# Kernel optimization log

Hardware: AMD Instinct MI355X
Metric: run time of the kernel (lower is better)

Reference implementation:

```python
import jax, jax.numpy as jnp
import numpy as np

B, T, D, H = 2, 2048, 1024, 16
DH = D // H


def setup_inputs() -> dict:
    key = jax.random.key(0)
    ks = jax.random.split(key, 5)
    scale = 1.0 / np.sqrt(D)
    return {
        "x": jax.random.normal(ks[0], (B, T, D), dtype=jnp.float32),
        "Wq": jax.random.normal(ks[1], (D, D), dtype=jnp.float32) * scale,
        "Wk": jax.random.normal(ks[2], (D, D), dtype=jnp.float32) * scale,
        "Wv": jax.random.normal(ks[3], (D, D), dtype=jnp.float32) * scale,
        "Wo": jax.random.normal(ks[4], (D, D), dtype=jnp.float32) * scale,
    }


def _split(y):
    # (B,T,D) -> (B,H,T,DH)
    b, t, _ = y.shape
    return y.reshape(b, t, H, DH).transpose(0, 2, 1, 3)


def reference(x, Wq, Wk, Wv, Wo):
    q = _split(x @ Wq)
    k = _split(x @ Wk)
    v = _split(x @ Wv)
    scores = jnp.einsum("bhqd,bhkd->bhqk", q, k) / jnp.sqrt(jnp.float32(DH))
    t = x.shape[1]
    # additive causal mask: -1e9 above the diagonal (matches band_part logic)
    causal = jnp.tril(jnp.ones((t, t), dtype=jnp.float32))
    scores = scores + (1.0 - causal) * -1e9
    attn = jax.nn.softmax(scores, axis=-1)
    out = jnp.einsum("bhqk,bhkd->bhqd", attn, v)  # (B,H,T,DH)
    out = out.transpose(0, 2, 1, 3).reshape(x.shape[0], t, D)
    return out @ Wo
```

## Files before the change

kernel.cpp:

```cpp
#include <hip/hip_runtime.h>

#define BB 2
#define TT 2048
#define DD 1024
#define HH 16
#define DHD 64
#define MM (BB*TT)

typedef __attribute__((ext_vector_type(8))) short short8;
typedef __attribute__((ext_vector_type(4))) float float4v;
typedef unsigned short u16;

__device__ inline float bf2f(u16 u) {
    union { unsigned int i; float f; } v;
    v.i = ((unsigned int)u) << 16;
    return v.f;
}
__device__ inline u16 f2bf(float f) {
    union { float f; unsigned int i; } v;
    v.f = f;
    unsigned int x = v.i;
    unsigned int r = (x + 0x7fffu + ((x >> 16) & 1u)) >> 16;
    return (u16)r;
}

__global__ __launch_bounds__(256) void prep_k(const float* __restrict__ x,
                                              const float* __restrict__ Wq,
                                              const float* __restrict__ Wk,
                                              const float* __restrict__ Wv,
                                              const float* __restrict__ Wo,
                                              u16* __restrict__ xb,
                                              u16* __restrict__ WT) {
    int tid = threadIdx.x;
    if (blockIdx.z == 4) {
        int bid = blockIdx.y * 32 + blockIdx.x;
#pragma unroll
        for (int k = 0; k < 4; k++) {
            int i = bid * 1024 + k * 256 + tid;
            float4v v = ((const float4v*)x)[i];
            ushort4 o;
            o.x = f2bf(v[0]); o.y = f2bf(v[1]); o.z = f2bf(v[2]); o.w = f2bf(v[3]);
            ((ushort4*)xb)[i] = o;
        }
        return;
    }
    __shared__ u16 t[32][33];
    int wsel = blockIdx.z;
    const float* W = (wsel == 0) ? Wq : (wsel == 1) ? Wk : (wsel == 2) ? Wv : Wo;
    u16* o = WT + (size_t)wsel * DD * DD;
    int k0 = blockIdx.y * 32, n0 = blockIdx.x * 32;
    int tx = tid & 31, ty = tid >> 5;
#pragma unroll
    for (int i = 0; i < 4; i++) {
        int k = ty + i * 8;
        t[k][tx] = f2bf(W[(size_t)(k0 + k) * DD + n0 + tx]);
    }
    __syncthreads();
#pragma unroll
    for (int i = 0; i < 4; i++) {
        int n = ty + i * 8;
        o[(size_t)(n0 + n) * DD + k0 + tx] = t[tx][n];
    }
}

template <int MODE, int TM, int TN, int BK>
__global__ __launch_bounds__(256) void gemm_k(const u16* __restrict__ A,
                                              const u16* __restrict__ WT0,
                                              void* __restrict__ outp) {
    const int K = DD;
    const int MT = TM / 32, NT = TN / 32;
    const int NS = (TM + TN) * (BK / 8) / 256;
    const int CPR = BK / 8;

    int z = blockIdx.z;
    const u16* WT = WT0 + (size_t)z * DD * DD;
    int n0 = blockIdx.x * TN, m0 = blockIdx.y * TM;

    __shared__ u16 S[(TM + TN) * BK];

    int tid = threadIdx.x;
    int lane = tid & 63, w = tid >> 6;
    int wm = (w >> 1) * (TM / 2), wn = (w & 1) * (TN / 2);
    int quad = lane >> 4, l16 = lane & 15;

    const u16* gp[NS];
    u16* lp[NS];
#pragma unroll
    for (int j = 0; j < NS; j++) {
        int cid = tid + j * 256;
        int r = cid / CPR, c = cid % CPR;
        lp[j] = S + r * BK + (c ^ (r & 7)) * 8;
        gp[j] = (r < TM ? A + (size_t)(m0 + r) * K
                        : WT + (size_t)(n0 + r - TM) * K) + c * 8;
    }
    int swz = l16 & 7;

    float4v acc[MT][NT];
#pragma unroll
    for (int i = 0; i < MT; i++)
#pragma unroll
        for (int j = 0; j < NT; j++) acc[i][j] = (float4v)(0.0f);

    short8 pr[NS];
#pragma unroll
    for (int j = 0; j < NS; j++) pr[j] = *(const short8*)gp[j];

    const int NK = K / BK;
#pragma unroll 1
    for (int ki = 0; ki < NK; ki++) {
        __syncthreads();
#pragma unroll
        for (int j = 0; j < NS; j++) *(short8*)lp[j] = pr[j];
        __syncthreads();

        if (ki + 1 < NK) {
            int k0 = (ki + 1) * BK;
#pragma unroll
            for (int j = 0; j < NS; j++) pr[j] = *(const short8*)(gp[j] + k0);
        }

#pragma unroll
        for (int ks = 0; ks < BK / 32; ks++) {
            int cq = ((ks * 4 + quad) ^ swz) * 8;
            short8 a[MT], b[NT];
#pragma unroll
            for (int mt = 0; mt < MT; mt++)
                a[mt] = *(const short8*)&S[(wm + mt * 16 + l16) * BK + cq];
#pragma unroll
            for (int nt = 0; nt < NT; nt++)
                b[nt] = *(const short8*)&S[(TM + wn + nt * 16 + l16) * BK + cq];
#pragma unroll
            for (int mt = 0; mt < MT; mt++)
#pragma unroll
                for (int nt = 0; nt < NT; nt++)
                    acc[mt][nt] = __builtin_amdgcn_mfma_f32_16x16x32_bf16(
                        a[mt], b[nt], acc[mt][nt], 0, 0, 0);
        }
    }

#pragma unroll
    for (int mt = 0; mt < MT; mt++) {
#pragma unroll
        for (int nt = 0; nt < NT; nt++) {
#pragma unroll
            for (int r = 0; r < 4; r++) {
                int m = m0 + wm + mt * 16 + quad * 4 + r;
                int n = n0 + wn + nt * 16 + l16;
                float v = acc[mt][nt][r];
                if constexpr (MODE == 0) {
                    int bb = m >> 11, t = m & 2047;
                    int h = n >> 6, dh = n & 63;
                    size_t idx;
                    if (z == 2)
                        idx = (((size_t)2 * BB * HH + bb * HH + h) * DHD + dh) * TT + t;
                    else
                        idx = (((size_t)z * BB * HH + bb * HH + h) * TT + t) * DHD + dh;
                    ((u16*)outp)[idx] = f2bf(v);
                } else {
                    ((float*)outp)[(size_t)m * DD + n] = v;
                }
            }
        }
    }
}

__global__ __launch_bounds__(512) void attn_k(const u16* __restrict__ QKV,
                                              u16* __restrict__ AO) {
    const u16* Q  = QKV;
    const u16* Kp = QKV + (size_t)MM * DD;
    const u16* Vp = QKV + (size_t)2 * MM * DD;
    int bh = blockIdx.x;
    int qt = 31 - blockIdx.y;
    size_t hoff = (size_t)bh * TT * DHD;

    __shared__ u16 Ks[2][2][64 * 64];
    __shared__ u16 VTs[2][2][64 * 64];
    __shared__ u16 Ps[8][16 * 64];

    int tid = threadIdx.x;
    int lane = tid & 63, wv = tid >> 6;
    int g = wv >> 2, w4 = wv & 3;
    int quad = lane >> 4, l16 = lane & 15;
    int cxs = l16 & 7;

    int sr = tid >> 3, sc = tid & 7;
    int sl = sr * 64 + ((sc ^ (sr & 7)) * 8);
    const u16* gK = Kp + hoff + (size_t)sr * DHD + sc * 8;
    const u16* gV = Vp + hoff + (size_t)sr * TT + sc * 8;

    u16* Qstage = &Ps[0][0];

    const float qscale = 0.125f * 1.4426950408889634f;
    int q0 = qt * 64;
    {
        short8 v = *(const short8*)(Q + hoff + (size_t)(q0 + sr) * DHD + sc * 8);
        short8 sv;
#pragma unroll
        for (int e = 0; e < 8; e++) sv[e] = (short)f2bf(bf2f((u16)v[e]) * qscale);
        *(short8*)&Qstage[sl] = sv;
    }

    short8 prK[2], prV[2];
    prK[0] = *(const short8*)gK;
    prK[1] = *(const short8*)(gK + (size_t)64 * DHD);
    prV[0] = *(const short8*)gV;
    prV[1] = *(const short8*)(gV + 64);

    __syncthreads();
    int fr = w4 * 16 + l16;
    short8 aq0 = *(const short8*)&Qstage[fr * 64 + ((quad ^ cxs) * 8)];
    short8 aq1 = *(const short8*)&Qstage[fr * 64 + (((4 + quad) ^ cxs) * 8)];

    int NR = (qt >> 1) + 1;

    float4v o[4];
#pragma unroll
    for (int i = 0; i < 4; i++) o[i] = (float4v)(0.0f);
    float lr = 0.0f;

#pragma unroll 1
    for (int jt = 0; jt < NR; jt++) {
        int db = jt & 1;
#pragma unroll
        for (int tt = 0; tt < 2; tt++) {
            *(short8*)&Ks[db][tt][sl]  = prK[tt];
            *(short8*)&VTs[db][tt][sl] = prV[tt];
        }
        __syncthreads();

        if (jt + 1 < NR) {
            size_t nj = (size_t)(jt + 1) * 128;
            prK[0] = *(const short8*)(gK + nj * DHD);
            prK[1] = *(const short8*)(gK + (nj + 64) * DHD);
            prV[0] = *(const short8*)(gV + nj);
            prV[1] = *(const short8*)(gV + nj + 64);
        }

        int tj = 2 * jt + g;
        if (tj <= qt) {
            float4v s[4];
#pragma unroll
            for (int ct = 0; ct < 4; ct++) {
                int kr = (ct * 16 + l16) * 64;
                short8 ak0 = *(const short8*)&Ks[db][g][kr + ((quad ^ cxs) * 8)];
                short8 ak1 = *(const short8*)&Ks[db][g][kr + (((4 + quad) ^ cxs) * 8)];
                float4v sv = (float4v)(0.0f);
                sv = __builtin_amdgcn_mfma_f32_16x16x32_bf16(ak0, aq0, sv, 0, 0, 0);
                sv = __builtin_amdgcn_mfma_f32_16x16x32_bf16(ak1, aq1, sv, 0, 0, 0);
                s[ct] = sv;
            }

            if (tj == qt) {
                int ql = w4 * 16 + l16;
#pragma unroll
                for (int ct = 0; ct < 4; ct++)
#pragma unroll
                    for (int r = 0; r < 4; r++) {
                        int kvl = ct * 16 + quad * 4 + r;
                        if (kvl > ql) s[ct][r] = -30000.0f;
                    }
            }

#pragma unroll
            for (int ct = 0; ct < 4; ct++) {
                float p0 = __builtin_amdgcn_exp2f(s[ct][0]);
                float p1 = __builtin_amdgcn_exp2f(s[ct][1]);
                float p2 = __builtin_amdgcn_exp2f(s[ct][2]);
                float p3 = __builtin_amdgcn_exp2f(s[ct][3]);
                lr += (p0 + p1) + (p2 + p3);
                union { float f; unsigned u; } c0, c1, c2, c3;
                c0.f = p0; c1.f = p1; c2.f = p2; c3.f = p3;
                ushort4 pw;
                pw.x = (u16)(c0.u >> 16);
                pw.y = (u16)(c1.u >> 16);
                pw.z = (u16)(c2.u >> 16);
                pw.w = (u16)(c3.u >> 16);
                int chnk = (ct * 2 + (quad >> 1)) ^ cxs;
                *(ushort4*)&Ps[wv][l16 * 64 + chnk * 8 + (quad & 1) * 4] = pw;
            }

            short8 ap0 = *(const short8*)&Ps[wv][l16 * 64 + ((quad ^ cxs) * 8)];
            short8 ap1 = *(const short8*)&Ps[wv][l16 * 64 + (((4 + quad) ^ cxs) * 8)];
#pragma unroll
            for (int ct = 0; ct < 4; ct++) {
                int vr = (ct * 16 + l16) * 64;
                short8 bv0 = *(const short8*)&VTs[db][g][vr + ((quad ^ cxs) * 8)];
                short8 bv1 = *(const short8*)&VTs[db][g][vr + (((4 + quad) ^ cxs) * 8)];
                o[ct] = __builtin_amdgcn_mfma_f32_16x16x32_bf16(ap0, bv0, o[ct], 0, 0, 0);
                o[ct] = __builtin_amdgcn_mfma_f32_16x16x32_bf16(ap1, bv1, o[ct], 0, 0, 0);
            }
        }
    }

    __syncthreads();
    float* Of = (float*)&Ks[0][0][0];
    float* Lf = (float*)&VTs[0][0][0];
    if (g == 1) {
#pragma unroll
        for (int ct = 0; ct < 4; ct++)
#pragma unroll
            for (int r = 0; r < 4; r++)
                Of[(((w4 * 4 + ct) * 4 + r) * 64) + lane] = o[ct][r];
        Lf[w4 * 64 + lane] = lr;
    }
    __syncthreads();
    if (g == 0) {
#pragma unroll
        for (int ct = 0; ct < 4; ct++)
#pragma unroll
            for (int r = 0; r < 4; r++)
                o[ct][r] += Of[(((w4 * 4 + ct) * 4 + r) * 64) + lane];
        lr += Lf[w4 * 64 + lane];

        float rs = lr;
        rs += __shfl_xor(rs, 16);
        rs += __shfl_xor(rs, 32);
        int gbase = lane & 48;
        float rinv[4];
#pragma unroll
        for (int r = 0; r < 4; r++)
            rinv[r] = 1.0f / __shfl(rs, gbase + quad * 4 + r);

        int b = bh >> 4, h = bh & 15;
#pragma unroll
        for (int ct = 0; ct < 4; ct++) {
#pragma unroll
            for (int r = 0; r < 4; r++) {
                int q = q0 + w4 * 16 + quad * 4 + r;
                int d = h * 64 + ct * 16 + l16;
                AO[(size_t)(b * TT + q) * DD + d] = f2bf(o[ct][r] * rinv[r]);
            }
        }
    }
}

extern "C" void kernel_launch(void* const* d_in, const int* in_sizes, int n_in,
                              void* d_out, int out_size, void* d_ws, size_t ws_size,
                              hipStream_t stream) {
    const float* x  = (const float*)d_in[0];
    const float* Wq = (const float*)d_in[1];
    const float* Wk = (const float*)d_in[2];
    const float* Wv = (const float*)d_in[3];
    const float* Wo = (const float*)d_in[4];

    u16* xb  = (u16*)d_ws;
    u16* WT  = xb + (size_t)MM * DD;
    u16* QKV = WT + (size_t)4 * DD * DD;
    u16* AO  = QKV + (size_t)3 * MM * DD;
    float* out = (float*)d_out;

    prep_k<<<dim3(32, 32, 5), 256, 0, stream>>>(x, Wq, Wk, Wv, Wo, xb, WT);
    gemm_k<0, 128, 128, 64><<<dim3(DD / 128, MM / 128, 3), 256, 0, stream>>>(xb, WT, QKV);
    attn_k<<<dim3(32, 32), 512, 0, stream>>>(QKV, AO);
    gemm_k<1, 64, 128, 64><<<dim3(DD / 128, MM / 64, 1), 256, 0, stream>>>(AO, WT + (size_t)3 * DD * DD, out);
}
```

Measured before the change: 169.7 us.

## Restructure attention to 4 waves per block with direct-global V loads

The attention kernel drops from 8 waves, where two groups split KV tiles and reduce through shared memory, to 4 waves that each walk every KV tile sequentially. This removes the cross-group reduction and its extra barriers. V fragments are now read straight from global memory into registers instead of being staged in LDS, and Q staging becomes per-wave with no block barrier. The cost is less intra-block parallelism and more uncoalesced, possibly redundant global V reads, in exchange for lower LDS use and potentially higher occupancy.

```diff
diff --git a/kernel.cpp b/kernel.cpp
--- a/kernel.cpp
+++ b/kernel.cpp
@@ -164,7 +164,7 @@
     }
 }
 
-__global__ __launch_bounds__(512) void attn_k(const u16* __restrict__ QKV,
+__global__ __launch_bounds__(256) void attn_k(const u16* __restrict__ QKV,
                                               u16* __restrict__ AO) {
     const u16* Q  = QKV;
     const u16* Kp = QKV + (size_t)MM * DD;
@@ -173,163 +173,135 @@
     int qt = 31 - blockIdx.y;
     size_t hoff = (size_t)bh * TT * DHD;
 
-    __shared__ u16 Ks[2][2][64 * 64];
-    __shared__ u16 VTs[2][2][64 * 64];
-    __shared__ u16 Ps[8][16 * 64];
+    __shared__ u16 Ks[2][64 * 64];
+    __shared__ u16 Ps[4][16 * 64];
 
     int tid = threadIdx.x;
     int lane = tid & 63, wv = tid >> 6;
-    int g = wv >> 2, w4 = wv & 3;
     int quad = lane >> 4, l16 = lane & 15;
     int cxs = l16 & 7;
 
-    int sr = tid >> 3, sc = tid & 7;
-    int sl = sr * 64 + ((sc ^ (sr & 7)) * 8);
-    const u16* gK = Kp + hoff + (size_t)sr * DHD + sc * 8;
-    const u16* gV = Vp + hoff + (size_t)sr * TT + sc * 8;
-
-    u16* Qstage = &Ps[0][0];
+    int r0 = tid >> 3, c0 = tid & 7;
+    int sl0 = r0 * 64 + ((c0 ^ (r0 & 7)) * 8);
+    const u16* gK = Kp + hoff + (size_t)r0 * DHD + c0 * 8;
 
     const float qscale = 0.125f * 1.4426950408889634f;
     int q0 = qt * 64;
-    {
-        short8 v = *(const short8*)(Q + hoff + (size_t)(q0 + sr) * DHD + sc * 8);
+    u16* Qs = &Ps[wv][0];
+#pragma unroll
+    for (int c = 0; c < 2; c++) {
+        int pp = lane + 64 * c;
+        int qr = pp >> 3, qc = pp & 7;
+        short8 v = *(const short8*)(Q + hoff + (size_t)(q0 + wv * 16 + qr) * DHD + qc * 8);
         short8 sv;
 #pragma unroll
         for (int e = 0; e < 8; e++) sv[e] = (short)f2bf(bf2f((u16)v[e]) * qscale);
-        *(short8*)&Qstage[sl] = sv;
-    }
-
-    short8 prK[2], prV[2];
-    prK[0] = *(const short8*)gK;
-    prK[1] = *(const short8*)(gK + (size_t)64 * DHD);
-    prV[0] = *(const short8*)gV;
-    prV[1] = *(const short8*)(gV + 64);
-
-    __syncthreads();
-    int fr = w4 * 16 + l16;
-    short8 aq0 = *(const short8*)&Qstage[fr * 64 + ((quad ^ cxs) * 8)];
-    short8 aq1 = *(const short8*)&Qstage[fr * 64 + (((4 + quad) ^ cxs) * 8)];
-
-    int NR = (qt >> 1) + 1;
-
+        *(short8*)&Qs[qr * 64 + ((qc ^ (qr & 7)) * 8)] = sv;
+    }
+    short8 aq0 = *(const short8*)&Qs[l16 * 64 + ((quad ^ cxs) * 8)];
+    short8 aq1 = *(const short8*)&Qs[l16 * 64 + (((4 + quad) ^ cxs) * 8)];
+
+    const u16* gV0 = Vp + hoff + (size_t)l16 * TT + quad * 8;
+
+    short8 prK0 = *(const short8*)gK;
+    short8 prK1 = *(const short8*)(gK + 32 * DHD);
+
+    const int NTL = qt + 1;
     float4v o[4];
 #pragma unroll
     for (int i = 0; i < 4; i++) o[i] = (float4v)(0.0f);
     float lr = 0.0f;
 
 #pragma unroll 1
-    for (int jt = 0; jt < NR; jt++) {
-        int db = jt & 1;
-#pragma unroll
-        for (int tt = 0; tt < 2; tt++) {
-            *(short8*)&Ks[db][tt][sl]  = prK[tt];
-            *(short8*)&VTs[db][tt][sl] = prV[tt];
-        }
+    for (int tj = 0; tj < NTL; tj++) {
+        int db = tj & 1;
+        *(short8*)&Ks[db][sl0] = prK0;
+        *(short8*)&Ks[db][sl0 + 32 * 64] = prK1;
         __syncthreads();
 
-        if (jt + 1 < NR) {
-            size_t nj = (size_t)(jt + 1) * 128;
-            prK[0] = *(const short8*)(gK + nj * DHD);
-            prK[1] = *(const short8*)(gK + (nj + 64) * DHD);
-            prV[0] = *(const short8*)(gV + nj);
-            prV[1] = *(const short8*)(gV + nj + 64);
-        }
-
-        int tj = 2 * jt + g;
-        if (tj <= qt) {
-            float4v s[4];
+        if (tj + 1 < NTL) {
+            const u16* g = gK + (size_t)(tj + 1) * 64 * DHD;
+            prK0 = *(const short8*)g;
+            prK1 = *(const short8*)(g + 32 * DHD);
+        }
+
+        short8 bv0[4], bv1[4];
+        {
+            const u16* gv = gV0 + tj * 64;
 #pragma unroll
             for (int ct = 0; ct < 4; ct++) {
-                int kr = (ct * 16 + l16) * 64;
-                short8 ak0 = *(const short8*)&Ks[db][g][kr + ((quad ^ cxs) * 8)];
-                short8 ak1 = *(const short8*)&Ks[db][g][kr + (((4 + quad) ^ cxs) * 8)];
-                float4v sv = (float4v)(0.0f);
-                sv = __builtin_amdgcn_mfma_f32_16x16x32_bf16(ak0, aq0, sv, 0, 0, 0);
-                sv = __builtin_amdgcn_mfma_f32_16x16x32_bf16(ak1, aq1, sv, 0, 0, 0);
-                s[ct] = sv;
+                bv0[ct] = *(const short8*)(gv + (size_t)ct * 16 * TT);
+                bv1[ct] = *(const short8*)(gv + (size_t)ct * 16 * TT + 32);
             }
-
-            if (tj == qt) {
-                int ql = w4 * 16 + l16;
-#pragma unroll
-                for (int ct = 0; ct < 4; ct++)
-#pragma unroll
-                    for (int r = 0; r < 4; r++) {
-                        int kvl = ct * 16 + quad * 4 + r;
-                        if (kvl > ql) s[ct][r] = -30000.0f;
-                    }
-            }
-
-#pragma unroll
-            for (int ct = 0; ct < 4; ct++) {
-                float p0 = __builtin_amdgcn_exp2f(s[ct][0]);
-                float p1 = __builtin_amdgcn_exp2f(s[ct][1]);
-                float p2 = __builtin_amdgcn_exp2f(s[ct][2]);
-                float p3 = __builtin_amdgcn_exp2f(s[ct][3]);
-                lr += (p0 + p1) + (p2 + p3);
-                union { float f; unsigned u; } c0, c1, c2, c3;
-                c0.f = p0; c1.f = p1; c2.f = p2; c3.f = p3;
-                ushort4 pw;
-                pw.x = (u16)(c0.u >> 16);
-                pw.y = (u16)(c1.u >> 16);
-                pw.z = (u16)(c2.u >> 16);
-                pw.w = (u16)(c3.u >> 16);
-                int chnk = (ct * 2 + (quad >> 1)) ^ cxs;
-                *(ushort4*)&Ps[wv][l16 * 64 + chnk * 8 + (quad & 1) * 4] = pw;
-            }
-
-            short8 ap0 = *(const short8*)&Ps[wv][l16 * 64 + ((quad ^ cxs) * 8)];
-            short8 ap1 = *(const short8*)&Ps[wv][l16 * 64 + (((4 + quad) ^ cxs) * 8)];
-#pragma unroll
-            for (int ct = 0; ct < 4; ct++) {
-                int vr = (ct * 16 + l16) * 64;
-                short8 bv0 = *(const short8*)&VTs[db][g][vr + ((quad ^ cxs) * 8)];
-                short8 bv1 = *(const short8*)&VTs[db][g][vr + (((4 + quad) ^ cxs) * 8)];
-                o[ct] = __builtin_amdgcn_mfma_f32_16x16x32_bf16(ap0, bv0, o[ct], 0, 0, 0);
-                o[ct] = __builtin_amdgcn_mfma_f32_16x16x32_bf16(ap1, bv1, o[ct], 0, 0, 0);
-            }
-        }
-    }
-
-    __syncthreads();
-    float* Of = (float*)&Ks[0][0][0];
-    float* Lf = (float*)&VTs[0][0][0];
-    if (g == 1) {
-#pragma unroll
-        for (int ct = 0; ct < 4; ct++)
-#pragma unroll
-            for (int r = 0; r < 4; r++)
-                Of[(((w4 * 4 + ct) * 4 + r) * 64) + lane] = o[ct][r];
-        Lf[w4 * 64 + lane] = lr;
-    }
-    __syncthreads();
-    if (g == 0) {
-#pragma unroll
-        for (int ct = 0; ct < 4; ct++)
-#pragma unroll
-            for (int r = 0; r < 4; r++)
-                o[ct][r] += Of[(((w4 * 4 + ct) * 4 + r) * 64) + lane];
-        lr += Lf[w4 * 64 + lane];
-
-        float rs = lr;
-        rs += __shfl_xor(rs, 16);
-        rs += __shfl_xor(rs, 32);
-        int gbase = lane & 48;
-        float rinv[4];
-#pragma unroll
-        for (int r = 0; r < 4; r++)
-            rinv[r] = 1.0f / __shfl(rs, gbase + quad * 4 + r);
-
-        int b = bh >> 4, h = bh & 15;
+        }
+
+        float4v s[4];
 #pragma unroll
         for (int ct = 0; ct < 4; ct++) {
-#pragma unroll
-            for (int r = 0; r < 4; r++) {
-                int q = q0 + w4 * 16 + quad * 4 + r;
-                int d = h * 64 + ct * 16 + l16;
-                AO[(size_t)(b * TT + q) * DD + d] = f2bf(o[ct][r] * rinv[r]);
-            }
+            int kr = (ct * 16 + l16) * 64;
+            short8 ak0 = *(const short8*)&Ks[db][kr + ((quad ^ cxs) * 8)];
+            short8 ak1 = *(const short8*)&Ks[db][kr + (((4 + quad) ^ cxs) * 8)];
+            float4v sv = (float4v)(0.0f);
+            sv = __builtin_amdgcn_mfma_f32_16x16x32_bf16(ak0, aq0, sv, 0, 0, 0);
+            sv = __builtin_amdgcn_mfma_f32_16x16x32_bf16(ak1, aq1, sv, 0, 0, 0);
+            s[ct] = sv;
+        }
+
+        if (tj == qt) {
+            int ql = wv * 16 + l16;
+#pragma unroll
+            for (int ct = 0; ct < 4; ct++)
+#pragma unroll
+                for (int r = 0; r < 4; r++) {
+                    int kvl = ct * 16 + quad * 4 + r;
+                    if (kvl > ql) s[ct][r] = -30000.0f;
+                }
+        }
+
+#pragma unroll
+        for (int ct = 0; ct < 4; ct++) {
+            float p0 = __builtin_amdgcn_exp2f(s[ct][0]);
+            float p1 = __builtin_amdgcn_exp2f(s[ct][1]);
+            float p2 = __builtin_amdgcn_exp2f(s[ct][2]);
+            float p3 = __builtin_amdgcn_exp2f(s[ct][3]);
+            lr += (p0 + p1) + (p2 + p3);
+            union { float f; unsigned u; } c0_, c1_, c2_, c3_;
+            c0_.f = p0; c1_.f = p1; c2_.f = p2; c3_.f = p3;
+            ushort4 pw;
+            pw.x = (u16)(c0_.u >> 16);
+            pw.y = (u16)(c1_.u >> 16);
+            pw.z = (u16)(c2_.u >> 16);
+            pw.w = (u16)(c3_.u >> 16);
+            int chnk = (ct * 2 + (quad >> 1)) ^ cxs;
+            *(ushort4*)&Ps[wv][l16 * 64 + chnk * 8 + (quad & 1) * 4] = pw;
+        }
+
+        short8 ap0 = *(const short8*)&Ps[wv][l16 * 64 + ((quad ^ cxs) * 8)];
+        short8 ap1 = *(const short8*)&Ps[wv][l16 * 64 + (((4 + quad) ^ cxs) * 8)];
+#pragma unroll
+        for (int ct = 0; ct < 4; ct++) {
+            o[ct] = __builtin_amdgcn_mfma_f32_16x16x32_bf16(ap0, bv0[ct], o[ct], 0, 0, 0);
+            o[ct] = __builtin_amdgcn_mfma_f32_16x16x32_bf16(ap1, bv1[ct], o[ct], 0, 0, 0);
+        }
+    }
+
+    float rs = lr;
+    rs += __shfl_xor(rs, 16);
+    rs += __shfl_xor(rs, 32);
+    int gbase = lane & 48;
+    float rinv[4];
+#pragma unroll
+    for (int r = 0; r < 4; r++)
+        rinv[r] = 1.0f / __shfl(rs, gbase + quad * 4 + r);
+
+    int b = bh >> 4, h = bh & 15;
+#pragma unroll
+    for (int ct = 0; ct < 4; ct++) {
+#pragma unroll
+        for (int r = 0; r < 4; r++) {
+            int q = q0 + wv * 16 + quad * 4 + r;
+            int d = h * 64 + ct * 16 + l16;
+            AO[(size_t)(b * TT + q) * DD + d] = f2bf(o[ct][r] * rinv[r]);
         }
     }
 }
@@ -351,6 +323,6 @@
 
     prep_k<<<dim3(32, 32, 5), 256, 0, stream>>>(x, Wq, Wk, Wv, Wo, xb, WT);
     gemm_k<0, 128, 128, 64><<<dim3(DD / 128, MM / 128, 3), 256, 0, stream>>>(xb, WT, QKV);
-    attn_k<<<dim3(32, 32), 512, 0, stream>>>(QKV, AO);
+    attn_k<<<dim3(32, 32), 256, 0, stream>>>(QKV, AO);
     gemm_k<1, 64, 128, 64><<<dim3(DD / 128, MM / 64, 1), 256, 0, stream>>>(AO, WT + (size_t)3 * DD * DD, out);
 }
```

Measured after the change: 214.6 us. +26.4%, slower.
